# Optimization experiments

Measured on AMD Instinct MI355X. Metric: run time of the kernel, lower is better.

The kernel has to match this reference:

```python
import jax, jax.numpy as jnp
import numpy as np

N_NODES = 100000
N_EDGES = 3200000
D_IN, D_HID, D_OUT = 128, 128, 40


def _sage_conv(x, src, dst, W_l, W_r, b, counts):
    # mean aggregation of neighbor (source) features at destination nodes
    agg = jax.ops.segment_sum(x[src], dst, num_segments=N_NODES)  # [N, d]
    agg = agg / counts  # mean (isolated nodes stay zero via clamped counts)
    # PyG SAGEConv: out = lin_l(aggr) + lin_r(x_root); bias lives in lin_l
    return agg @ W_l + x @ W_r + b


def setup_inputs() -> dict:
    key = jax.random.key(0)
    ks = jax.random.split(key, 8)
    x = jax.random.normal(ks[0], (N_NODES, D_IN), dtype=jnp.float32)
    edge_index = jax.random.randint(ks[1], (2, N_EDGES), 0, N_NODES, dtype=jnp.int64)
    s1 = 1.0 / np.sqrt(D_IN)
    s2 = 1.0 / np.sqrt(D_HID)
    return {
        "x": x,
        "edge_index": edge_index,
        "W1_l": jax.random.uniform(ks[2], (D_IN, D_HID), jnp.float32, -s1, s1),
        "W1_r": jax.random.uniform(ks[3], (D_IN, D_HID), jnp.float32, -s1, s1),
        "b1": jnp.zeros((D_HID,), jnp.float32),
        "W2_l": jax.random.uniform(ks[4], (D_HID, D_OUT), jnp.float32, -s2, s2),
        "W2_r": jax.random.uniform(ks[5], (D_HID, D_OUT), jnp.float32, -s2, s2),
        "b2": jnp.zeros((D_OUT,), jnp.float32),
    }


def reference(x, edge_index, W1_l, W1_r, b1, W2_l, W2_r, b2):
    src, dst = edge_index[0], edge_index[1]
    # in-degree per destination node, clamped to avoid div-by-zero
    deg = jax.ops.segment_sum(jnp.ones((N_EDGES,), jnp.float32), dst, num_segments=N_NODES)
    counts = jnp.maximum(deg, 1.0)[:, None]  # [N, 1]
    h = jax.nn.relu(_sage_conv(x, src, dst, W1_l, W1_r, b1, counts))
    h = _sage_conv(h, src, dst, W2_l, W2_r, b2, counts)
    return jax.nn.log_softmax(h, axis=1)
```

## Files before the change

kernel.cpp:

```cpp
#include <hip/hip_runtime.h>
#include <hip/hip_bf16.h>
#include <hip/hip_fp8.h>
#include <math.h>

#define N_NODES 100000
#define D_IN    128
#define D_HID   128
#define D_OUT   40
#define NBUCK   391
#define CHUNK   4096
#define SLABCAP 16320
#define CAST_BLOCKS 6250


using short8  = __attribute__((ext_vector_type(8))) short;
using float4v = __attribute__((ext_vector_type(4))) float;
using floatx2 = __attribute__((ext_vector_type(2))) float;

__device__ __forceinline__ unsigned short f2b(float f) {
    __hip_bfloat16 b = __float2bfloat16(f);
    return *(unsigned short*)&b;
}
__device__ __forceinline__ unsigned packb(float a, float b) {
    return (unsigned)f2b(a) | ((unsigned)f2b(b) << 16);
}

__device__ __forceinline__ unsigned char f2q(float f) {
    __hip_fp8_e4m3 v(f);
    return *(unsigned char*)&v;
}
template <int SEL>
__device__ __forceinline__ float q2f(unsigned u) {
#if __has_builtin(__builtin_amdgcn_cvt_f32_fp8)
    return __builtin_amdgcn_cvt_f32_fp8((int)u, SEL);
#else
    unsigned char b = (u >> (SEL * 8)) & 0xff;
    __hip_fp8_e4m3 v;
    *(unsigned char*)&v = b;
    return (float)v;
#endif
}
template <bool HI>
__device__ __forceinline__ floatx2 pkcvt(unsigned u) {
#if __has_builtin(__builtin_amdgcn_cvt_pk_f32_fp8)
    return __builtin_amdgcn_cvt_pk_f32_fp8((int)u, HI);
#else
    floatx2 r;
    if constexpr (HI) { r[0] = q2f<2>(u); r[1] = q2f<3>(u); }
    else              { r[0] = q2f<0>(u); r[1] = q2f<1>(u); }
    return r;
#endif
}

__device__ __forceinline__ long long edge_at(const void* ei, int is64, long long idx) {
    if (is64) return ((const long long*)ei)[idx];
    return (long long)((const int*)ei)[idx];
}

__global__ __launch_bounds__(256) void prep_kernel(const float* __restrict__ x,
                                                   unsigned short* __restrict__ xb,
                                                   unsigned char* __restrict__ xq,
                                                   const float* __restrict__ W1l,
                                                   const float* __restrict__ W1r,
                                                   const float* __restrict__ W2l,
                                                   const float* __restrict__ W2r,
                                                   unsigned short* __restrict__ wp1,
                                                   unsigned short* __restrict__ wp2,
                                                   const int* __restrict__ ei,
                                                   int* __restrict__ flag,
                                                   unsigned* __restrict__ bcount) {
    const int b = blockIdx.x;
    if (b < CAST_BLOCKS) {
        long long i = ((long long)b * 256 + threadIdx.x) * 8;
        if (i >= (long long)N_NODES * 128) return;
        float4 a = *(const float4*)&x[i];
        float4 c = *(const float4*)&x[i + 4];
        ushort4 o0, o1;
        o0.x = f2b(a.x); o0.y = f2b(a.y); o0.z = f2b(a.z); o0.w = f2b(a.w);
        o1.x = f2b(c.x); o1.y = f2b(c.y); o1.z = f2b(c.z); o1.w = f2b(c.w);
        *(ushort4*)&xb[i] = o0;
        *(ushort4*)&xb[i + 4] = o1;
        uint2 p;
        p.x = (unsigned)f2q(a.x) | ((unsigned)f2q(a.y) << 8)
            | ((unsigned)f2q(a.z) << 16) | ((unsigned)f2q(a.w) << 24);
        p.y = (unsigned)f2q(c.x) | ((unsigned)f2q(c.y) << 8)
            | ((unsigned)f2q(c.z) << 16) | ((unsigned)f2q(c.w) << 24);
        *(uint2*)&xq[i] = p;
    } else if (b < CAST_BLOCKS + 21) {
        int t = (b - CAST_BLOCKS) * 256 + threadIdx.x;
        if (t < 4096) {
            int lane = t & 63;
            int ks = (t >> 6) & 7;
            int ct = t >> 9;
            int n = ct * 16 + (lane & 15);
            int kr = (lane >> 4) * 8;
            unsigned short v[8];
#pragma unroll
            for (int j = 0; j < 8; ++j) {
                int k = ks * 32 + kr + j;
                float f = (k < 128) ? W1l[k * 128 + n] : W1r[(k - 128) * 128 + n];
                v[j] = f2b(f);
            }
            ushort4 o0 = {v[0], v[1], v[2], v[3]};
            ushort4 o1 = {v[4], v[5], v[6], v[7]};
            *(ushort4*)&wp1[t * 8] = o0;
            *(ushort4*)&wp1[t * 8 + 4] = o1;
        } else if (t < 4096 + 1280) {
            int u = t - 4096;
            int lane = u & 63;
            int ks = (u >> 6) & 3;
            int ct = u >> 8;
            int n = ct * 16 + (lane & 15);
            int kr = (lane >> 4) * 8;
            unsigned short v[8];
#pragma unroll
            for (int j = 0; j < 8; ++j) {
                int k = ks * 32 + kr + j;
                float f = (n < 40) ? W2l[k * 40 + n] : W2r[k * 40 + (n - 40)];
                v[j] = f2b(f);
            }
            ushort4 o0 = {v[0], v[1], v[2], v[3]};
            ushort4 o1 = {v[4], v[5], v[6], v[7]};
            *(ushort4*)&wp2[u * 8] = o0;
            *(ushort4*)&wp2[u * 8 + 4] = o1;
        }
    } else {
        const int t = threadIdx.x;
        if (t < 64) {
            int ok = 1;
#pragma unroll
            for (int k = 0; k < 4; ++k) {
                if (ei[2 * (t * 4 + k) + 1] != 0) ok = 0;
            }
            int all0 = __all(ok);
            if (t == 0) *flag = all0 ? 1 : 0;
        }
        if (t < NBUCK) bcount[t] = 0u;
        if (t + 256 < NBUCK) bcount[t + 256] = 0u;
    }
}

__global__ __launch_bounds__(1024) void partition_kernel(const void* __restrict__ ei,
                                                         const int* __restrict__ flag,
                                                         unsigned* __restrict__ bcount,
                                                         unsigned* __restrict__ slab,
                                                         long long E) {
    __shared__ unsigned hist[NBUCK];
    __shared__ unsigned lstart[NBUCK];
    __shared__ unsigned gofs[NBUCK];
    __shared__ unsigned s[512];
    __shared__ unsigned rec[CHUNK];
    __shared__ unsigned short bkt[CHUNK];

    const int tid = threadIdx.x;
    const int is64 = *flag;
    const long long cb = (long long)blockIdx.x * CHUNK;
    const unsigned n = (unsigned)(((E - cb) < (long long)CHUNK) ? (E - cb) : CHUNK);

    if (tid < NBUCK) hist[tid] = 0;
    __syncthreads();

#pragma unroll
    for (int j = 0; j < CHUNK / 1024; ++j) {
        unsigned e = j * 1024 + tid;
        if (e < n) {
            unsigned d = (unsigned)edge_at(ei, is64, E + cb + e);
            atomicAdd(&hist[d >> 8], 1u);
        }
    }
    __syncthreads();

    if (tid < 512) s[tid] = (tid < NBUCK) ? hist[tid] : 0u;
    __syncthreads();
    for (int off = 1; off < 512; off <<= 1) {
        unsigned t = 0;
        if (tid < 512 && tid >= off) t = s[tid - off];
        __syncthreads();
        if (tid < 512) s[tid] += t;
        __syncthreads();
    }
    if (tid < NBUCK) {
        unsigned cnt = hist[tid];
        unsigned ex = s[tid] - cnt;
        lstart[tid] = ex;
        if (cnt) {
            unsigned g = atomicAdd(&bcount[tid], cnt);
            gofs[tid] = (unsigned)(tid * SLABCAP) + g - ex;
        }
        hist[tid] = 0;
    }
    __syncthreads();

#pragma unroll
    for (int j = 0; j < CHUNK / 1024; ++j) {
        unsigned e = j * 1024 + tid;
        if (e < n) {
            unsigned sv = (unsigned)edge_at(ei, is64, cb + e);
            unsigned d  = (unsigned)edge_at(ei, is64, E + cb + e);
            unsigned b = d >> 8;
            unsigned loc = atomicAdd(&hist[b], 1u);
            unsigned slot = lstart[b] + loc;
            rec[slot] = ((d & 255u) << 17) | sv;
            bkt[slot] = (unsigned short)b;
        }
    }
    __syncthreads();

#pragma unroll
    for (int j = 0; j < CHUNK / 1024; ++j) {
        unsigned i = j * 1024 + tid;
        if (i < n) {
            unsigned b = bkt[i];
            slab[gofs[b] + i] = rec[i];
        }
    }
}

__global__ __launch_bounds__(256) void build_kernel(const unsigned* __restrict__ slab,
                                                    const unsigned* __restrict__ bcount,
                                                    unsigned* __restrict__ deg,
                                                    float* __restrict__ invc,
                                                    unsigned* __restrict__ row_start,
                                                    int* __restrict__ csr) {
    __shared__ unsigned red[256];
    __shared__ unsigned cnt[256];
    __shared__ unsigned scn[256];
    const int tid = threadIdx.x;
    const int nb = blockIdx.x << 8;
    const long long sb = (long long)blockIdx.x * SLABCAP;

    {
        unsigned pv = 0;
        for (unsigned i = tid; i < (unsigned)blockIdx.x; i += 256) pv += bcount[i];
        red[tid] = pv;
        __syncthreads();
        for (int off = 128; off >= 1; off >>= 1) {
            if (tid < off) red[tid] += red[tid + off];
            __syncthreads();
        }
    }
    const unsigned es = red[0];
    const unsigned n  = bcount[blockIdx.x];

    cnt[tid] = 0;
    __syncthreads();
    for (unsigned i = tid; i < n; i += 256) {
        unsigned d = slab[sb + i] >> 17;
        atomicAdd(&cnt[d], 1u);
    }
    __syncthreads();
    unsigned v = cnt[tid];
    scn[tid] = v;
    __syncthreads();
    for (int off = 1; off < 256; off <<= 1) {
        unsigned t = (tid >= off) ? scn[tid - off] : 0u;
        __syncthreads();
        scn[tid] += t;
        __syncthreads();
    }
    unsigned ex = scn[tid] - v;
    int node = nb + tid;
    if (node < N_NODES) {
        deg[node] = v;
        invc[node] = 1.0f / fmaxf((float)v, 1.0f);
        row_start[node] = es + ex;
    }
    __syncthreads();
    cnt[tid] = ex;
    __syncthreads();
    for (unsigned i = tid; i < n; i += 256) {
        unsigned pr = slab[sb + i];
        unsigned d = pr >> 17;
        unsigned pos = es + atomicAdd(&cnt[d], 1u);
        csr[pos] = (int)(pr & 0x1FFFFu);
    }
}

__global__ __launch_bounds__(256) void gather_fp8_kernel(const unsigned char* __restrict__ featq,
                                                         const int* __restrict__ csr,
                                                         const unsigned* __restrict__ row_start,
                                                         const unsigned* __restrict__ deg,
                                                         const float* __restrict__ invc,
                                                         unsigned short* __restrict__ aggb) {
    const int wave = threadIdx.x >> 6;
    const int lane = threadIdx.x & 63;
    const int node = blockIdx.x * 4 + wave;
    if (node >= N_NODES) return;

    const unsigned start = row_start[node];
    const unsigned cnt = deg[node];
    const int s = lane >> 4;
    const unsigned cgo = (unsigned)((lane & 15) * 8);

    floatx2 acc[4];
#pragma unroll
    for (int k = 0; k < 4; ++k) acc[k] = (floatx2){0.f, 0.f};

    for (unsigned base = 0; base < cnt; base += 64) {
        unsigned rem = cnt - base;
        if (rem > 64u) rem = 64u;
        int nid = (lane < (int)rem) ? csr[start + base + lane] : 0;
        for (unsigned j = 0; j < rem; j += 8) {
            uint2 u0 = {0u, 0u}, u1 = {0u, 0u};
            unsigned i0 = j + s;
            unsigned i1 = j + 4 + s;
            int s0 = __shfl(nid, (int)(i0 & 63));
            int s1 = __shfl(nid, (int)(i1 & 63));
            if (i0 < rem) u0 = *(const uint2*)&featq[((unsigned)s0 << 7) + cgo];
            if (i1 < rem) u1 = *(const uint2*)&featq[((unsigned)s1 << 7) + cgo];
            acc[0] += pkcvt<false>(u0.x); acc[1] += pkcvt<true>(u0.x);
            acc[2] += pkcvt<false>(u0.y); acc[3] += pkcvt<true>(u0.y);
            acc[0] += pkcvt<false>(u1.x); acc[1] += pkcvt<true>(u1.x);
            acc[2] += pkcvt<false>(u1.y); acc[3] += pkcvt<true>(u1.y);
        }
    }

#pragma unroll
    for (int k = 0; k < 4; ++k) {
        acc[k][0] += __shfl_xor(acc[k][0], 16);
        acc[k][1] += __shfl_xor(acc[k][1], 16);
        acc[k][0] += __shfl_xor(acc[k][0], 32);
        acc[k][1] += __shfl_xor(acc[k][1], 32);
    }

    if (lane < 16) {
        const float ic = invc[node];
        uint4 o;
        o.x = packb(acc[0][0] * ic, acc[0][1] * ic);
        o.y = packb(acc[1][0] * ic, acc[1][1] * ic);
        o.z = packb(acc[2][0] * ic, acc[2][1] * ic);
        o.w = packb(acc[3][0] * ic, acc[3][1] * ic);
        *(uint4*)&aggb[(unsigned)node * 128u + cgo] = o;
    }
}

__global__ __launch_bounds__(256) void gemm12_kernel(const unsigned short* __restrict__ aggb,
                                                     const unsigned short* __restrict__ xb,
                                                     const unsigned short* __restrict__ wp1,
                                                     const float* __restrict__ b1,
                                                     const unsigned short* __restrict__ wp2,
                                                     const float* __restrict__ b2,
                                                     unsigned char* __restrict__ pq,
                                                     float* __restrict__ q) {
    __shared__ unsigned short sh[64][136];
    const int wave = threadIdx.x >> 6;
    const int lane = threadIdx.x & 63;
    const int row0 = blockIdx.x * 64 + wave * 16;
    const unsigned abase = (unsigned)(row0 + (lane & 15)) * 128u + (unsigned)((lane >> 4) * 8);

    float4v acc[8];
#pragma unroll
    for (int ct = 0; ct < 8; ++ct) acc[ct] = (float4v){0.f, 0.f, 0.f, 0.f};

#pragma unroll
    for (int ks = 0; ks < 8; ++ks) {
        union { uint4 u; short8 s; } af;
        if (ks < 4) af.u = *(const uint4*)&aggb[abase + ks * 32];
        else        af.u = *(const uint4*)&xb[abase + (ks - 4) * 32];
#pragma unroll
        for (int ct = 0; ct < 8; ++ct) {
            union { uint4 u; short8 s; } bf;
            bf.u = *(const uint4*)&wp1[((ct * 8 + ks) * 64 + lane) * 8];
            acc[ct] = __builtin_amdgcn_mfma_f32_16x16x32_bf16(af.s, bf.s, acc[ct], 0, 0, 0);
        }
    }

    const int lrow0 = wave * 16 + (lane >> 4) * 4;
    const int ccol = lane & 15;
#pragma unroll
    for (int ct = 0; ct < 8; ++ct) {
        const int col = ct * 16 + ccol;
        const float bv = b1[col];
#pragma unroll
        for (int r = 0; r < 4; ++r)
            sh[lrow0 + r][col] = f2b(fmaxf(acc[ct][r] + bv, 0.0f));
    }

    const unsigned short* aptr = &sh[wave * 16 + (lane & 15)][(lane >> 4) * 8];

    float4v acc2[5];
#pragma unroll
    for (int ct = 0; ct < 5; ++ct) acc2[ct] = (float4v){0.f, 0.f, 0.f, 0.f};

#pragma unroll
    for (int ks = 0; ks < 4; ++ks) {
        union { uint4 u; short8 s; } af;
        af.u = *(const uint4*)&aptr[ks * 32];
#pragma unroll
        for (int ct = 0; ct < 5; ++ct) {
            union { uint4 u; short8 s; } bf;
            bf.u = *(const uint4*)&wp2[((ct * 4 + ks) * 64 + lane) * 8];
            acc2[ct] = __builtin_amdgcn_mfma_f32_16x16x32_bf16(af.s, bf.s, acc2[ct], 0, 0, 0);
        }
    }

    const int crow0 = row0 + (lane >> 4) * 4;
#pragma unroll
    for (int ct = 0; ct < 5; ++ct) {
        const int col = ct * 16 + ccol;
#pragma unroll
        for (int r = 0; r < 4; ++r) {
            int row = crow0 + r;
            if (row < N_NODES) {
                if (col < D_OUT) {
                    pq[(unsigned)row * 40u + (unsigned)col] = f2q(acc2[ct][r]);
                } else {
                    q[(unsigned)row * 40u + (unsigned)(col - D_OUT)] = acc2[ct][r] + b2[col - D_OUT];
                }
            }
        }
    }
}

__global__ __launch_bounds__(256) void gather40_kernel(const unsigned char* __restrict__ pq,
                                                       const float* __restrict__ q,
                                                       const int* __restrict__ csr,
                                                       const unsigned* __restrict__ row_start,
                                                       const unsigned* __restrict__ deg,
                                                       const float* __restrict__ invc,
                                                       float* __restrict__ out) {
    __shared__ float sm[4][40];
    const int wave = threadIdx.x >> 6;
    const int lane = threadIdx.x & 63;
    const int node = blockIdx.x * 4 + wave;
    if (node >= N_NODES) return;

    const unsigned start = row_start[node];
    const unsigned cnt = deg[node];
    const int s = lane / 10;
    const int cg = lane % 10;
    const unsigned cgo = (unsigned)(cg * 4);
    const bool gactive = s < 6;

    floatx2 a01 = (floatx2){0.f, 0.f}, a23 = (floatx2){0.f, 0.f};

    for (unsigned base = 0; base < cnt; base += 64) {
        unsigned rem = cnt - base;
        if (rem > 64u) rem = 64u;
        int nid = (lane < (int)rem) ? csr[start + base + lane] : 0;
        for (unsigned j = 0; j < rem; j += 24) {
            unsigned u[4];
#pragma unroll
            for (int t = 0; t < 4; ++t) {
                unsigned idx = j + t * 6 + s;
                int sid = __shfl(nid, (int)(idx & 63));
                bool valid = gactive && (idx < rem);
                u[t] = valid ? *(const unsigned*)&pq[(unsigned)sid * 40u + cgo] : 0u;
            }
#pragma unroll
            for (int t = 0; t < 4; ++t) {
                a01 += pkcvt<false>(u[t]);
                a23 += pkcvt<true>(u[t]);
            }
        }
    }

    float a0 = a01[0], a1 = a01[1], a2 = a23[0], a3 = a23[1];
    {
        float t0, t1, t2, t3;
        t0 = __shfl(a0, lane + 30); t1 = __shfl(a1, lane + 30);
        t2 = __shfl(a2, lane + 30); t3 = __shfl(a3, lane + 30);
        if (lane < 30) { a0 += t0; a1 += t1; a2 += t2; a3 += t3; }
        t0 = __shfl(a0, lane + 20); t1 = __shfl(a1, lane + 20);
        t2 = __shfl(a2, lane + 20); t3 = __shfl(a3, lane + 20);
        if (lane < 10) { a0 += t0; a1 += t1; a2 += t2; a3 += t3; }
        t0 = __shfl(a0, lane + 10); t1 = __shfl(a1, lane + 10);
        t2 = __shfl(a2, lane + 10); t3 = __shfl(a3, lane + 10);
        if (lane < 10) { a0 += t0; a1 += t1; a2 += t2; a3 += t3; }
    }
    if (lane < 10) {
        sm[wave][cg * 4 + 0] = a0;
        sm[wave][cg * 4 + 1] = a1;
        sm[wave][cg * 4 + 2] = a2;
        sm[wave][cg * 4 + 3] = a3;
    }
    const bool active = lane < D_OUT;
    float v = active ? (sm[wave][active ? lane : 0] * invc[node]
                        + q[(unsigned)node * 40u + (unsigned)(active ? lane : 0)])
                     : -__builtin_huge_valf();
    float m = v;
#pragma unroll
    for (int off = 32; off >= 1; off >>= 1) m = fmaxf(m, __shfl_xor(m, off));
    float e = active ? expf(v - m) : 0.0f;
    float ssum = e;
#pragma unroll
    for (int off = 32; off >= 1; off >>= 1) ssum += __shfl_xor(ssum, off);
    float ls = logf(ssum);
    if (active) out[(unsigned)node * 40u + (unsigned)lane] = v - m - ls;
}

extern "C" void kernel_launch(void* const* d_in, const int* in_sizes, int n_in,
                              void* d_out, int out_size, void* d_ws, size_t ws_size,
                              hipStream_t stream) {
    const float* x   = (const float*)d_in[0];
    const void*  ei  = d_in[1];
    const float* W1l = (const float*)d_in[2];
    const float* W1r = (const float*)d_in[3];
    const float* b1  = (const float*)d_in[4];
    const float* W2l = (const float*)d_in[5];
    const float* W2r = (const float*)d_in[6];
    const float* b2  = (const float*)d_in[7];
    float* out = (float*)d_out;

    const long long E = (long long)in_sizes[1] / 2;
    const int NPB = (int)((E + CHUNK - 1) / CHUNK);

    char* ws = (char*)d_ws;
    int*      flag      = (int*)ws;
    unsigned* bcount    = (unsigned*)(ws + 4096);
    unsigned* deg       = (unsigned*)(ws + 16384);
    float*    invc      = (float*)(ws + 416384);
    unsigned* row_start = (unsigned*)(ws + 816384);
    int*      csr       = (int*)(ws + 1216384);
    unsigned short* xb  = (unsigned short*)(ws + 14016384);
    unsigned short* aggb= (unsigned short*)(ws + 39616384);
    unsigned* slab      = (unsigned*)(ws + 39616384);
    unsigned short* wp1 = (unsigned short*)(ws + 65216384);
    unsigned short* wp2 = (unsigned short*)(ws + 65281920);
    unsigned char*  pq  = (unsigned char*)(ws + 65310720);
    float*    q         = (float*)(ws + 69310720);
    unsigned char*  xq  = (unsigned char*)(ws + 90910720);

    prep_kernel<<<CAST_BLOCKS + 21 + 1, 256, 0, stream>>>(x, xb, xq, W1l, W1r, W2l, W2r,
                                                          wp1, wp2, (const int*)ei, flag, bcount);

    partition_kernel<<<NPB, 1024, 0, stream>>>(ei, flag, bcount, slab, E);
    build_kernel<<<NBUCK, 256, 0, stream>>>(slab, bcount, deg, invc, row_start, csr);

    gather_fp8_kernel<<<(N_NODES + 3) / 4, 256, 0, stream>>>(xq, csr, row_start, deg, invc, aggb);
    gemm12_kernel<<<(N_NODES + 63) / 64, 256, 0, stream>>>(aggb, xb, wp1, b1, wp2, b2, pq, q);

    gather40_kernel<<<(N_NODES + 3) / 4, 256, 0, stream>>>(pq, q, csr, row_start, deg, invc, out);
}
```

Baseline: 322.4 us.

## Use wave-shuffle scans in partition/build, split fp8 gather launch, shrink gather40 unroll

Replaces the shared-memory Hillis-Steele scans and tree reduction in the partition and build kernels with wavefront shuffle scans plus a small cross-wave combine, cutting many __syncthreads barriers. The fp8 gather is split into two launches over node halves. The gather40 inner loop processes 18 neighbors per iteration instead of 24, with 3 loads in flight instead of 4. The gather split adds launch overhead and the smaller unroll lowers memory-level parallelism, while the partition and build kernels mainly save barrier cost.

```diff
diff --git a/kernel.cpp b/kernel.cpp
--- a/kernel.cpp
+++ b/kernel.cpp
@@ -149,10 +149,13 @@
     __shared__ unsigned lstart[NBUCK];
     __shared__ unsigned gofs[NBUCK];
     __shared__ unsigned s[512];
+    __shared__ unsigned ws[16];
     __shared__ unsigned rec[CHUNK];
     __shared__ unsigned short bkt[CHUNK];
 
     const int tid = threadIdx.x;
+    const int lane = tid & 63;
+    const int w = tid >> 6;
     const int is64 = *flag;
     const long long cb = (long long)blockIdx.x * CHUNK;
     const unsigned n = (unsigned)(((E - cb) < (long long)CHUNK) ? (E - cb) : CHUNK);
@@ -170,14 +173,28 @@
     }
     __syncthreads();
 
-    if (tid < 512) s[tid] = (tid < NBUCK) ? hist[tid] : 0u;
-    __syncthreads();
-    for (int off = 1; off < 512; off <<= 1) {
-        unsigned t = 0;
-        if (tid < 512 && tid >= off) t = s[tid - off];
+    {
+        unsigned v0 = (tid < NBUCK) ? hist[tid] : 0u;
+        unsigned x = v0;
+#pragma unroll
+        for (int off = 1; off < 64; off <<= 1) {
+            unsigned t = __shfl_up(x, off);
+            if (lane >= off) x += t;
+        }
+        if (lane == 63) ws[w] = x;
         __syncthreads();
-        if (tid < 512) s[tid] += t;
+        if (w == 0) {
+            unsigned y = (lane < 16) ? ws[lane] : 0u;
+#pragma unroll
+            for (int off = 1; off < 16; off <<= 1) {
+                unsigned t = __shfl_up(y, off);
+                if (lane >= off) y += t;
+            }
+            if (lane < 16) ws[lane] = y;
+        }
         __syncthreads();
+        unsigned pre = (w > 0) ? ws[w - 1] : 0u;
+        if (tid < NBUCK) s[tid] = x + pre;
     }
     if (tid < NBUCK) {
         unsigned cnt = hist[tid];
@@ -222,24 +239,22 @@
                                                     float* __restrict__ invc,
                                                     unsigned* __restrict__ row_start,
                                                     int* __restrict__ csr) {
-    __shared__ unsigned red[256];
+    __shared__ unsigned red[4];
+    __shared__ unsigned ws[4];
     __shared__ unsigned cnt[256];
-    __shared__ unsigned scn[256];
     const int tid = threadIdx.x;
+    const int lane = tid & 63;
+    const int w = tid >> 6;
     const int nb = blockIdx.x << 8;
     const long long sb = (long long)blockIdx.x * SLABCAP;
 
-    {
-        unsigned pv = 0;
-        for (unsigned i = tid; i < (unsigned)blockIdx.x; i += 256) pv += bcount[i];
-        red[tid] = pv;
-        __syncthreads();
-        for (int off = 128; off >= 1; off >>= 1) {
-            if (tid < off) red[tid] += red[tid + off];
-            __syncthreads();
-        }
-    }
-    const unsigned es = red[0];
+    unsigned pv = 0;
+    for (unsigned i = tid; i < (unsigned)blockIdx.x; i += 256) pv += bcount[i];
+#pragma unroll
+    for (int off = 32; off >= 1; off >>= 1) pv += __shfl_xor(pv, off);
+    if (lane == 0) red[w] = pv;
+    __syncthreads();
+    const unsigned es = red[0] + red[1] + red[2] + red[3];
     const unsigned n  = bcount[blockIdx.x];
 
     cnt[tid] = 0;
@@ -250,15 +265,18 @@
     }
     __syncthreads();
     unsigned v = cnt[tid];
-    scn[tid] = v;
-    __syncthreads();
-    for (int off = 1; off < 256; off <<= 1) {
-        unsigned t = (tid >= off) ? scn[tid - off] : 0u;
-        __syncthreads();
-        scn[tid] += t;
-        __syncthreads();
-    }
-    unsigned ex = scn[tid] - v;
+    unsigned x = v;
+#pragma unroll
+    for (int off = 1; off < 64; off <<= 1) {
+        unsigned t = __shfl_up(x, off);
+        if (lane >= off) x += t;
+    }
+    if (lane == 63) ws[w] = x;
+    __syncthreads();
+    unsigned pre = 0;
+#pragma unroll
+    for (int k = 0; k < 4; ++k) if (k < w) pre += ws[k];
+    unsigned ex = x + pre - v;
     int node = nb + tid;
     if (node < N_NODES) {
         deg[node] = v;
@@ -281,11 +299,12 @@
                                                          const unsigned* __restrict__ row_start,
                                                          const unsigned* __restrict__ deg,
                                                          const float* __restrict__ invc,
-                                                         unsigned short* __restrict__ aggb) {
+                                                         unsigned short* __restrict__ aggb,
+                                                         int node0, int nend) {
     const int wave = threadIdx.x >> 6;
     const int lane = threadIdx.x & 63;
-    const int node = blockIdx.x * 4 + wave;
-    if (node >= N_NODES) return;
+    const int node = node0 + blockIdx.x * 4 + wave;
+    if (node >= nend) return;
 
     const unsigned start = row_start[node];
     const unsigned cnt = deg[node];
@@ -438,17 +457,17 @@
         unsigned rem = cnt - base;
         if (rem > 64u) rem = 64u;
         int nid = (lane < (int)rem) ? csr[start + base + lane] : 0;
-        for (unsigned j = 0; j < rem; j += 24) {
-            unsigned u[4];
-#pragma unroll
-            for (int t = 0; t < 4; ++t) {
+        for (unsigned j = 0; j < rem; j += 18) {
+            unsigned u[3];
+#pragma unroll
+            for (int t = 0; t < 3; ++t) {
                 unsigned idx = j + t * 6 + s;
                 int sid = __shfl(nid, (int)(idx & 63));
                 bool valid = gactive && (idx < rem);
                 u[t] = valid ? *(const unsigned*)&pq[(unsigned)sid * 40u + cgo] : 0u;
             }
 #pragma unroll
-            for (int t = 0; t < 4; ++t) {
+            for (int t = 0; t < 3; ++t) {
                 a01 += pkcvt<false>(u[t]);
                 a23 += pkcvt<true>(u[t]);
             }
@@ -527,7 +546,8 @@
     partition_kernel<<<NPB, 1024, 0, stream>>>(ei, flag, bcount, slab, E);
     build_kernel<<<NBUCK, 256, 0, stream>>>(slab, bcount, deg, invc, row_start, csr);
 
-    gather_fp8_kernel<<<(N_NODES + 3) / 4, 256, 0, stream>>>(xq, csr, row_start, deg, invc, aggb);
+    gather_fp8_kernel<<<12500, 256, 0, stream>>>(xq, csr, row_start, deg, invc, aggb, 0, 50000);
+    gather_fp8_kernel<<<12500, 256, 0, stream>>>(xq, csr, row_start, deg, invc, aggb, 50000, 100000);
     gemm12_kernel<<<(N_NODES + 63) / 64, 256, 0, stream>>>(aggb, xb, wp1, b1, wp2, b2, pq, q);
 
     gather40_kernel<<<(N_NODES + 3) / 4, 256, 0, stream>>>(pq, q, csr, row_start, deg, invc, out);
```

New measurement: 328.5 us. Within noise of the previous version (+1.9%).
